# Performance work log

Hardware: AMD Instinct MI355X
Metric: run time of the kernel (lower is better)

Reference implementation:

```python
import jax, jax.numpy as jnp
import numpy as np
from jax import lax

WINDOW_SIZE = 11
SIGMA = 1.5
DATA_RANGE = 1.0


def _gaussian_window(channels):
    coords = jnp.arange(WINDOW_SIZE, dtype=jnp.float32) - WINDOW_SIZE // 2
    g = jnp.exp(-coords ** 2 / (2.0 * SIGMA ** 2))
    g = g / g.sum()
    w2d = jnp.outer(g, g)
    w2d = w2d / w2d.sum()
    # depthwise kernel: (C, 1, K, K) in OIHW with feature_group_count=C
    return jnp.broadcast_to(w2d, (channels, 1, WINDOW_SIZE, WINDOW_SIZE))


def _dwconv(x, window, channels):
    pad = WINDOW_SIZE // 2
    return lax.conv_general_dilated(
        x, window,
        window_strides=(1, 1),
        padding=[(pad, pad), (pad, pad)],
        dimension_numbers=('NCHW', 'OIHW', 'NCHW'),
        feature_group_count=channels,
    )


def setup_inputs() -> dict:
    key = jax.random.key(0)
    k1, k2 = jax.random.split(key)
    B, C, H, W = 16, 3, 512, 512
    x = jax.random.uniform(k1, (B, C, H, W), dtype=jnp.float32)
    y = jax.random.uniform(k2, (B, C, H, W), dtype=jnp.float32)
    return {"x": x, "y": y}


def reference(x, y):
    channels = x.shape[1]
    window = _gaussian_window(channels)
    mu_x = _dwconv(x, window, channels)
    mu_y = _dwconv(y, window, channels)
    mu_x2 = mu_x * mu_x
    mu_y2 = mu_y * mu_y
    mu_xy = mu_x * mu_y
    sigma_x2 = _dwconv(x * x, window, channels) - mu_x2
    sigma_y2 = _dwconv(y * y, window, channels) - mu_y2
    sigma_xy = _dwconv(x * y, window, channels) - mu_xy
    c1 = (0.01 * DATA_RANGE) ** 2
    c2 = (0.03 * DATA_RANGE) ** 2
    ssim_map = (2 * mu_xy + c1) * (2 * sigma_xy + c2) / (
        (mu_x2 + mu_y2 + c1) * (sigma_x2 + sigma_y2 + c2) + 1e-08)
    per_image = ssim_map.mean(axis=(1, 2, 3))
    return 1.0 - per_image.mean()
```

## Files before the change

kernel.cpp:

```cpp
#include <hip/hip_runtime.h>
#include <math.h>


#define IMG_W 512
#define IMG_H 512
#define PLANES 48
#define TX 64
#define TYS 128
#define RAD 5
#define NT 256
#define GDX (IMG_W / TX)
#define GDY (IMG_H / TYS)
#define NBLK (GDX * GDY * PLANES)
#define NWAVES (NBLK * 4)
#define NCH 9
#define CSTR 40
#define PSTR (16 * CSTR)
#define WSTR (4 * PSTR)
#define NUMREC (IMG_W * IMG_H * 4)
#define CHSTEP (16 * IMG_W * 4)
#define INVW  0.26601181f
#define GC2   0.32059890f

typedef _Float16 h2 __attribute__((ext_vector_type(2)));
typedef _Float16 h4 __attribute__((ext_vector_type(4)));
typedef _Float16 h8 __attribute__((ext_vector_type(8)));
typedef float f32x4 __attribute__((ext_vector_type(4)));
typedef int i32x4 __attribute__((ext_vector_type(4)));

__device__ __forceinline__ i32x4 make_srd(const float* p) {
    union { i32x4 v; struct { const float* p; unsigned rng; unsigned cfg; } s; } u;
    u.s.p = p; u.s.rng = NUMREC; u.s.cfg = 0x00020000u;
    return u.v;
}

template<int N>
__device__ __forceinline__ void vwait() {
    asm volatile("s_waitcnt vmcnt(%0)" :: "n"(N) : "memory");
    __builtin_amdgcn_sched_barrier(0);
}

__device__ __forceinline__ float exp2_fast(float a) {
#if __has_builtin(__builtin_amdgcn_exp2f)
    return __builtin_amdgcn_exp2f(a);
#else
    return exp2f(a);
#endif
}

__device__ __forceinline__ float wbandf(int idx) {
    const float fd = (float)(idx - 5);
    const float g = exp2_fast(-(fd * fd) * GC2) * INVW;
    return ((unsigned)idx <= 10u) ? g : 0.f;
}

__device__ __forceinline__ h2 pkrtz(float a, float b) {
    auto t = __builtin_amdgcn_cvt_pkrtz(a, b);
    h2 r;
    __builtin_memcpy(&r, &t, sizeof(r));
    return r;
}

__device__ __forceinline__ h4 pack4(f32x4 a) {
    const h2 lo = pkrtz(a[0], a[1]), hi = pkrtz(a[2], a[3]);
    h4 v;
    v[0] = lo.x; v[1] = lo.y; v[2] = hi.x; v[3] = hi.y;
    return v;
}

__device__ __forceinline__ void hconv_chunk(
    f32x4 xa, f32x4 xb, f32x4 ya, f32x4 yb, h8 whB,
    _Float16* wp)
{
    const f32x4 zz = {0.f, 0.f, 0.f, 0.f};
    const h2 xh0 = pkrtz(xa[0], xa[1]), xh1 = pkrtz(xa[2], xa[3]);
    const h2 xh2 = pkrtz(xb[0], xb[1]), xh3 = pkrtz(xb[2], xb[3]);
    const h2 yh0 = pkrtz(ya[0], ya[1]), yh1 = pkrtz(ya[2], ya[3]);
    const h2 yh2 = pkrtz(yb[0], yb[1]), yh3 = pkrtz(yb[2], yb[3]);
    const h2 s0 = xh0 + yh0, s1 = xh1 + yh1, s2 = xh2 + yh2, s3 = xh3 + yh3;
    const h2 d0 = xh0 - yh0, d1 = xh1 - yh1, d2 = xh2 - yh2, d3 = xh3 - yh3;
    h8 sA, dA;
    sA[0] = s0.x; sA[1] = s0.y; sA[2] = s1.x; sA[3] = s1.y;
    sA[4] = s2.x; sA[5] = s2.y; sA[6] = s3.x; sA[7] = s3.y;
    dA[0] = d0.x; dA[1] = d0.y; dA[2] = d1.x; dA[3] = d1.y;
    dA[4] = d2.x; dA[5] = d2.y; dA[6] = d3.x; dA[7] = d3.y;
    const h8 s2A = sA * sA;
    const h8 d2A = dA * dA;
    const f32x4 hS  = __builtin_amdgcn_mfma_f32_16x16x32_f16(sA,  whB, zz, 0, 0, 0);
    const f32x4 hD  = __builtin_amdgcn_mfma_f32_16x16x32_f16(dA,  whB, zz, 0, 0, 0);
    const f32x4 hS2 = __builtin_amdgcn_mfma_f32_16x16x32_f16(s2A, whB, zz, 0, 0, 0);
    const f32x4 hD2 = __builtin_amdgcn_mfma_f32_16x16x32_f16(d2A, whB, zz, 0, 0, 0);
    *(h4*)(wp + 0 * PSTR) = pack4(hS);
    *(h4*)(wp + 1 * PSTR) = pack4(hD);
    *(h4*)(wp + 2 * PSTR) = pack4(hS2);
    *(h4*)(wp + 3 * PSTR) = pack4(hD2);
}

__device__ __forceinline__ float mapsum(f32x4 aS, f32x4 aD, f32x4 aS2, f32x4 aD2,
                                        float cv)
{
    float local = 0.f;
    #pragma unroll
    for (int r = 0; r < 4; ++r) {
        const float mS = aS[r]  * cv, mD = aD[r]  * cv;
        const float eS = aS2[r] * cv, eD = aD2[r] * cv;
        const float ms2 = mS * mS, md2 = mD * mD;
        const float Pm = 0.5f * (ms2 - md2);
        const float Qm = 0.5f * (ms2 + md2);
        const float Pe = 0.5f * (eS - eD);
        const float Qe = 0.5f * (eS + eD);
        const float c1 = 1e-4f, c2 = 9e-4f;
        const float num = (Pm + c1) * (Pe - Pm + c2);
        const float den = (Qm + c1) * (Qe - Qm + c2) + 1e-8f;
        local += num * __builtin_amdgcn_rcpf(den);
    }
    return local;
}

#define MFMA16(A, B, C) __builtin_amdgcn_mfma_f32_16x16x32_f16((A), (B), (C), 0, 0, 0)

#define ISSUE(slot) do {                                                      \
    asm volatile("buffer_load_dwordx4 %0, %1, %2, 0 offen"                    \
                 : "=v"(LXA[slot]) : "v"(voff), "s"(srdx));                   \
    asm volatile("buffer_load_dwordx4 %0, %1, %2, 0 offen offset:16"          \
                 : "=v"(LXB[slot]) : "v"(voff), "s"(srdx));                   \
    asm volatile("buffer_load_dwordx4 %0, %1, %2, 0 offen"                    \
                 : "=v"(LYA[slot]) : "v"(voff), "s"(srdy));                   \
    asm volatile("buffer_load_dwordx4 %0, %1, %2, 0 offen offset:16"          \
                 : "=v"(LYB[slot]) : "v"(voff), "s"(srdy));                   \
    voff += CHSTEP;                                                           \
} while (0)

#define VCONV(C) do {                                                         \
    const _Float16* rp = rbase + ((((C) + qh) & 1) << 4);                     \
    const h8 B0 = *(const h8*)(rp + 0 * PSTR);           \
    const h8 B1 = *(const h8*)(rp + 1 * PSTR);                                \
    const h8 B2 = *(const h8*)(rp + 2 * PSTR);                                \
    const h8 B3 = *(const h8*)(rp + 3 * PSTR);                                \
    const f32x4 aS  = MFMA16(wvA, B0, zz);                                    \
    const f32x4 aD  = MFMA16(wvA, B1, zz);                                    \
    const f32x4 aS2 = MFMA16(wvA, B2, zz);                                    \
    const f32x4 aD2 = MFMA16(wvA, B3, zz);                                    \
    local += mapsum(aS, aD, aS2, aD2, cv);                                    \
} while (0)

__global__ __launch_bounds__(NT, 4) void ssim_tile_kernel(
    const float* __restrict__ x, const float* __restrict__ y,
    float* __restrict__ partials)
{
    __shared__ __align__(16) _Float16 Ht[4 * WSTR];

    const int tid = threadIdx.x;
    const int l = tid & 63, wid = tid >> 6;
    const int q = l >> 4, fc = l & 15;
    const int ql = q & 1, qh = q >> 1;

    const int plane = blockIdx.z;
    const i32x4 srdx = make_srd(x + (size_t)plane * IMG_H * IMG_W);
    const i32x4 srdy = make_srd(y + (size_t)plane * IMG_H * IMG_W);
    const int C0 = blockIdx.x * TX;
    const int R0 = blockIdx.y * TYS;
    const int c0 = 16 * wid;
    const int gcol = C0 + c0 - 8 + 8 * q;
    int voff = ((unsigned)gcol < (unsigned)IMG_W)
             ? (((R0 - RAD + fc) << 11) + (gcol << 2)) : 0x60000000;

    f32x4 LXA[3], LXB[3], LYA[3], LYB[3];
    ISSUE(0); ISSUE(1); ISSUE(2);

    float s2w = 0.f;
    #pragma unroll
    for (int k = 0; k <= 10; ++k) s2w += (float)(_Float16)wbandf(k);
    const float cv = 1.f / (s2w * s2w);

    h8 whB, wvA;
    #pragma unroll
    for (int e = 0; e < 8; ++e) {
        whB[e] = (_Float16)wbandf(8 * q + e - fc - 3);
        wvA[e] = (_Float16)wbandf(8 * q + e - fc);
    }

    _Float16* const Hw = Ht + wid * WSTR;
    _Float16* const hwr = Hw + fc * CSTR + 4 * q;
    const _Float16* const rbase = Hw + fc * CSTR + 8 * ql;

    const f32x4 zz = {0.f, 0.f, 0.f, 0.f};
    float local = 0.f;

    #pragma unroll
    for (int c = 0; c < NCH; ++c) {
        if (c >= 2) VCONV(c);
        if (c <= 6) vwait<8>();
        else if (c == 7) vwait<4>();
        else vwait<0>();
        hconv_chunk(LXA[c % 3], LXB[c % 3], LYA[c % 3], LYB[c % 3],
                    whB, hwr + ((c & 1) << 4));
        if (c + 3 < NCH) ISSUE(c % 3);
    }

    VCONV(9);

    #pragma unroll
    for (int off = 32; off > 0; off >>= 1)
        local += __shfl_down(local, off, 64);
    const int gid = (blockIdx.x + GDX * (blockIdx.y + GDY * blockIdx.z)) * 4 + wid;
    if (l == 0) partials[gid] = local;
}

__global__ __launch_bounds__(256) void ssim_finalize_kernel(
    const float* __restrict__ partials, float* __restrict__ out)
{
    const int tid = threadIdx.x;
    double s = 0.0;
    #pragma unroll 4
    for (int i = tid; i < NWAVES; i += 256) s += (double)partials[i];
    #pragma unroll
    for (int off = 32; off > 0; off >>= 1)
        s += __shfl_down(s, off, 64);
    __shared__ double ws_[256 / 64];
    const int lane = tid & 63, wv = tid >> 6;
    if (lane == 0) ws_[wv] = s;
    __syncthreads();
    if (tid == 0) {
        const double t = ws_[0] + ws_[1] + ws_[2] + ws_[3];
        const double n = (double)PLANES * IMG_H * IMG_W;
        out[0] = (float)(1.0 - t / n);
    }
}

extern "C" void kernel_launch(void* const* d_in, const int* in_sizes, int n_in,
                              void* d_out, int out_size, void* d_ws, size_t ws_size,
                              hipStream_t stream)
{
    const float* x = (const float*)d_in[0];
    const float* y = (const float*)d_in[1];
    float* out = (float*)d_out;
    float* partials = (float*)d_ws;

    dim3 grid(GDX, GDY, PLANES);
    ssim_tile_kernel<<<grid, NT, 0, stream>>>(x, y, partials);
    ssim_finalize_kernel<<<1, 256, 0, stream>>>(partials, out);
}
```

Before: 131.2 us.

## Fuse final reduction into tile kernel via atomics and last-block finalize

Removes the separate finalize kernel launch. Each block now reduces its four wave sums in shared memory, adds them atomically into a double accumulator, and the last block to finish, found through an atomic counter, writes the output. A memset is added before the launch to zero the accumulator and counter. The global loads also gain an sc0 cache-policy bit. The double atomics add contention and make the summation order nondeterministic, and the memset is an extra stream operation.

```diff
diff --git a/kernel.cpp b/kernel.cpp
--- a/kernel.cpp
+++ b/kernel.cpp
@@ -12,7 +12,6 @@
 #define GDX (IMG_W / TX)
 #define GDY (IMG_H / TYS)
 #define NBLK (GDX * GDY * PLANES)
-#define NWAVES (NBLK * 4)
 #define NCH 9
 #define CSTR 40
 #define PSTR (16 * CSTR)
@@ -120,13 +119,13 @@
 #define MFMA16(A, B, C) __builtin_amdgcn_mfma_f32_16x16x32_f16((A), (B), (C), 0, 0, 0)
 
 #define ISSUE(slot) do {                                                      \
-    asm volatile("buffer_load_dwordx4 %0, %1, %2, 0 offen"                    \
+    asm volatile("buffer_load_dwordx4 %0, %1, %2, 0 offen sc0"                \
                  : "=v"(LXA[slot]) : "v"(voff), "s"(srdx));                   \
-    asm volatile("buffer_load_dwordx4 %0, %1, %2, 0 offen offset:16"          \
+    asm volatile("buffer_load_dwordx4 %0, %1, %2, 0 offen offset:16 sc0"      \
                  : "=v"(LXB[slot]) : "v"(voff), "s"(srdx));                   \
-    asm volatile("buffer_load_dwordx4 %0, %1, %2, 0 offen"                    \
+    asm volatile("buffer_load_dwordx4 %0, %1, %2, 0 offen sc0"                \
                  : "=v"(LYA[slot]) : "v"(voff), "s"(srdy));                   \
-    asm volatile("buffer_load_dwordx4 %0, %1, %2, 0 offen offset:16"          \
+    asm volatile("buffer_load_dwordx4 %0, %1, %2, 0 offen offset:16 sc0"      \
                  : "=v"(LYB[slot]) : "v"(voff), "s"(srdy));                   \
     voff += CHSTEP;                                                           \
 } while (0)
@@ -146,9 +145,11 @@
 
 __global__ __launch_bounds__(NT, 4) void ssim_tile_kernel(
     const float* __restrict__ x, const float* __restrict__ y,
-    float* __restrict__ partials)
+    double* __restrict__ acc, unsigned* __restrict__ cnt,
+    float* __restrict__ out)
 {
     __shared__ __align__(16) _Float16 Ht[4 * WSTR];
+    __shared__ float wave_sums[NT / 64];
 
     const int tid = threadIdx.x;
     const int l = tid & 63, wid = tid >> 6;
@@ -203,28 +204,19 @@
     #pragma unroll
     for (int off = 32; off > 0; off >>= 1)
         local += __shfl_down(local, off, 64);
-    const int gid = (blockIdx.x + GDX * (blockIdx.y + GDY * blockIdx.z)) * 4 + wid;
-    if (l == 0) partials[gid] = local;
-}
-
-__global__ __launch_bounds__(256) void ssim_finalize_kernel(
-    const float* __restrict__ partials, float* __restrict__ out)
-{
-    const int tid = threadIdx.x;
-    double s = 0.0;
-    #pragma unroll 4
-    for (int i = tid; i < NWAVES; i += 256) s += (double)partials[i];
-    #pragma unroll
-    for (int off = 32; off > 0; off >>= 1)
-        s += __shfl_down(s, off, 64);
-    __shared__ double ws_[256 / 64];
-    const int lane = tid & 63, wv = tid >> 6;
-    if (lane == 0) ws_[wv] = s;
+    if (l == 0) wave_sums[wid] = local;
     __syncthreads();
     if (tid == 0) {
-        const double t = ws_[0] + ws_[1] + ws_[2] + ws_[3];
-        const double n = (double)PLANES * IMG_H * IMG_W;
-        out[0] = (float)(1.0 - t / n);
+        const double s = (double)wave_sums[0] + (double)wave_sums[1]
+                       + (double)wave_sums[2] + (double)wave_sums[3];
+        atomicAdd(acc, s);
+        __threadfence();
+        const unsigned t = atomicAdd(cnt, 1u);
+        if (t == NBLK - 1) {
+            const double tot = atomicAdd(acc, 0.0);
+            const double n = (double)PLANES * IMG_H * IMG_W;
+            out[0] = (float)(1.0 - tot / n);
+        }
     }
 }
 
@@ -235,9 +227,11 @@
     const float* x = (const float*)d_in[0];
     const float* y = (const float*)d_in[1];
     float* out = (float*)d_out;
-    float* partials = (float*)d_ws;
+    double* acc = (double*)d_ws;
+    unsigned* cnt = (unsigned*)((char*)d_ws + 8);
+
+    hipMemsetAsync(d_ws, 0, 16, stream);
 
     dim3 grid(GDX, GDY, PLANES);
-    ssim_tile_kernel<<<grid, NT, 0, stream>>>(x, y, partials);
-    ssim_finalize_kernel<<<1, 256, 0, stream>>>(partials, out);
-}
+    ssim_tile_kernel<<<grid, NT, 0, stream>>>(x, y, acc, cnt, out);
+}
```

Result: slower. 196.8 us (+50.0%).

## Stage input tile cooperatively in LDS to remove redundant halo loads

Applied to the files above, without the earlier changes.

Each block now loads its 16-row chunk of x and y (including the column halo) once, cooperatively, into a double-buffered LDS staging area as fp16 sum/difference, instead of each wave loading its own overlapping 32-column slice. The horizontal MFMA pass then reads from LDS. This removes duplicated global loads across the four waves. In exchange it adds a __syncthreads per chunk and drops the three-deep register prefetch to a single chunk in flight, with a full vwait<0> each iteration, which may expose memory latency. Partials are also reduced per block rather than per wave.

```diff
diff --git a/kernel.cpp b/kernel.cpp
--- a/kernel.cpp
+++ b/kernel.cpp
@@ -12,8 +12,9 @@
 #define GDX (IMG_W / TX)
 #define GDY (IMG_H / TYS)
 #define NBLK (GDX * GDY * PLANES)
-#define NWAVES (NBLK * 4)
 #define NCH 9
+#define SC4 20
+#define SSTR 88
 #define CSTR 40
 #define PSTR (16 * CSTR)
 #define WSTR (4 * PSTR)
@@ -66,34 +67,6 @@
     h4 v;
     v[0] = lo.x; v[1] = lo.y; v[2] = hi.x; v[3] = hi.y;
     return v;
-}
-
-__device__ __forceinline__ void hconv_chunk(
-    f32x4 xa, f32x4 xb, f32x4 ya, f32x4 yb, h8 whB,
-    _Float16* wp)
-{
-    const f32x4 zz = {0.f, 0.f, 0.f, 0.f};
-    const h2 xh0 = pkrtz(xa[0], xa[1]), xh1 = pkrtz(xa[2], xa[3]);
-    const h2 xh2 = pkrtz(xb[0], xb[1]), xh3 = pkrtz(xb[2], xb[3]);
-    const h2 yh0 = pkrtz(ya[0], ya[1]), yh1 = pkrtz(ya[2], ya[3]);
-    const h2 yh2 = pkrtz(yb[0], yb[1]), yh3 = pkrtz(yb[2], yb[3]);
-    const h2 s0 = xh0 + yh0, s1 = xh1 + yh1, s2 = xh2 + yh2, s3 = xh3 + yh3;
-    const h2 d0 = xh0 - yh0, d1 = xh1 - yh1, d2 = xh2 - yh2, d3 = xh3 - yh3;
-    h8 sA, dA;
-    sA[0] = s0.x; sA[1] = s0.y; sA[2] = s1.x; sA[3] = s1.y;
-    sA[4] = s2.x; sA[5] = s2.y; sA[6] = s3.x; sA[7] = s3.y;
-    dA[0] = d0.x; dA[1] = d0.y; dA[2] = d1.x; dA[3] = d1.y;
-    dA[4] = d2.x; dA[5] = d2.y; dA[6] = d3.x; dA[7] = d3.y;
-    const h8 s2A = sA * sA;
-    const h8 d2A = dA * dA;
-    const f32x4 hS  = __builtin_amdgcn_mfma_f32_16x16x32_f16(sA,  whB, zz, 0, 0, 0);
-    const f32x4 hD  = __builtin_amdgcn_mfma_f32_16x16x32_f16(dA,  whB, zz, 0, 0, 0);
-    const f32x4 hS2 = __builtin_amdgcn_mfma_f32_16x16x32_f16(s2A, whB, zz, 0, 0, 0);
-    const f32x4 hD2 = __builtin_amdgcn_mfma_f32_16x16x32_f16(d2A, whB, zz, 0, 0, 0);
-    *(h4*)(wp + 0 * PSTR) = pack4(hS);
-    *(h4*)(wp + 1 * PSTR) = pack4(hD);
-    *(h4*)(wp + 2 * PSTR) = pack4(hS2);
-    *(h4*)(wp + 3 * PSTR) = pack4(hD2);
 }
 
 __device__ __forceinline__ float mapsum(f32x4 aS, f32x4 aD, f32x4 aS2, f32x4 aD2,
@@ -119,16 +92,30 @@
 
 #define MFMA16(A, B, C) __builtin_amdgcn_mfma_f32_16x16x32_f16((A), (B), (C), 0, 0, 0)
 
-#define ISSUE(slot) do {                                                      \
+#define ISSUE() do {                                                          \
     asm volatile("buffer_load_dwordx4 %0, %1, %2, 0 offen"                    \
-                 : "=v"(LXA[slot]) : "v"(voff), "s"(srdx));                   \
-    asm volatile("buffer_load_dwordx4 %0, %1, %2, 0 offen offset:16"          \
-                 : "=v"(LXB[slot]) : "v"(voff), "s"(srdx));                   \
+                 : "=v"(X0) : "v"(voff0), "s"(srdx));                         \
     asm volatile("buffer_load_dwordx4 %0, %1, %2, 0 offen"                    \
-                 : "=v"(LYA[slot]) : "v"(voff), "s"(srdy));                   \
-    asm volatile("buffer_load_dwordx4 %0, %1, %2, 0 offen offset:16"          \
-                 : "=v"(LYB[slot]) : "v"(voff), "s"(srdy));                   \
-    voff += CHSTEP;                                                           \
+                 : "=v"(Y0) : "v"(voff0), "s"(srdy));                         \
+    if (has1) {                                                               \
+        asm volatile("buffer_load_dwordx4 %0, %1, %2, 0 offen"                \
+                     : "=v"(X1) : "v"(voff1), "s"(srdx));                     \
+        asm volatile("buffer_load_dwordx4 %0, %1, %2, 0 offen"                \
+                     : "=v"(Y1) : "v"(voff1), "s"(srdy));                     \
+    }                                                                         \
+    voff0 += CHSTEP; voff1 += CHSTEP;                                         \
+} while (0)
+
+#define STAGE_WRITE(X, Y, ROW, C4, SLOT) do {                                 \
+    const h2 xl = pkrtz((X)[0], (X)[1]), xh = pkrtz((X)[2], (X)[3]);          \
+    const h2 yl = pkrtz((Y)[0], (Y)[1]), yh = pkrtz((Y)[2], (Y)[3]);          \
+    const h2 sl = xl + yl, sh = xh + yh;                                      \
+    const h2 dl = xl - yl, dh = xh - yh;                                      \
+    h4 sv, dv;                                                                \
+    sv[0] = sl.x; sv[1] = sl.y; sv[2] = sh.x; sv[3] = sh.y;                   \
+    dv[0] = dl.x; dv[1] = dl.y; dv[2] = dh.x; dv[3] = dh.y;                   \
+    *(h4*)&sdIn[SLOT][0][ROW][4 * (C4)] = sv;                                 \
+    *(h4*)&sdIn[SLOT][1][ROW][4 * (C4)] = dv;                                 \
 } while (0)
 
 #define VCONV(C) do {                                                         \
@@ -148,7 +135,9 @@
     const float* __restrict__ x, const float* __restrict__ y,
     float* __restrict__ partials)
 {
+    __shared__ _Float16 sdIn[2][2][16][SSTR];
     __shared__ __align__(16) _Float16 Ht[4 * WSTR];
+    __shared__ float wave_sums[NT / 64];
 
     const int tid = threadIdx.x;
     const int l = tid & 63, wid = tid >> 6;
@@ -161,12 +150,20 @@
     const int C0 = blockIdx.x * TX;
     const int R0 = blockIdx.y * TYS;
     const int c0 = 16 * wid;
-    const int gcol = C0 + c0 - 8 + 8 * q;
-    int voff = ((unsigned)gcol < (unsigned)IMG_W)
-             ? (((R0 - RAD + fc) << 11) + (gcol << 2)) : 0x60000000;
-
-    f32x4 LXA[3], LXB[3], LYA[3], LYB[3];
-    ISSUE(0); ISSUE(1); ISSUE(2);
+
+    const int row0 = tid / SC4, c40 = tid - SC4 * row0;
+    const bool has1 = tid < 320 - NT;
+    const int p1 = NT + tid;
+    const int row1 = p1 / SC4, c41 = p1 - SC4 * row1;
+    const int gcol0 = C0 - 8 + 4 * c40;
+    const int gcol1 = C0 - 8 + 4 * c41;
+    int voff0 = ((unsigned)gcol0 < (unsigned)IMG_W)
+              ? (((R0 - RAD + row0) << 11) + (gcol0 << 2)) : 0x60000000;
+    int voff1 = ((unsigned)gcol1 < (unsigned)IMG_W)
+              ? (((R0 - RAD + row1) << 11) + (gcol1 << 2)) : 0x60000000;
+
+    f32x4 X0, Y0, X1, Y1;
+    ISSUE();
 
     float s2w = 0.f;
     #pragma unroll
@@ -189,13 +186,29 @@
 
     #pragma unroll
     for (int c = 0; c < NCH; ++c) {
+        vwait<0>();
+        STAGE_WRITE(X0, Y0, row0, c40, c & 1);
+        if (has1) STAGE_WRITE(X1, Y1, row1, c41, c & 1);
+        if (c + 1 < NCH) ISSUE();
+        __syncthreads();
+
         if (c >= 2) VCONV(c);
-        if (c <= 6) vwait<8>();
-        else if (c == 7) vwait<4>();
-        else vwait<0>();
-        hconv_chunk(LXA[c % 3], LXB[c % 3], LYA[c % 3], LYB[c % 3],
-                    whB, hwr + ((c & 1) << 4));
-        if (c + 3 < NCH) ISSUE(c % 3);
+
+        {
+            const h8 sA = *(const h8*)&sdIn[c & 1][0][fc][c0 + 8 * q];
+            const h8 dA = *(const h8*)&sdIn[c & 1][1][fc][c0 + 8 * q];
+            const h8 s2A = sA * sA;
+            const h8 d2A = dA * dA;
+            const f32x4 hS  = MFMA16(sA,  whB, zz);
+            const f32x4 hD  = MFMA16(dA,  whB, zz);
+            const f32x4 hS2 = MFMA16(s2A, whB, zz);
+            const f32x4 hD2 = MFMA16(d2A, whB, zz);
+            _Float16* wp = hwr + ((c & 1) << 4);
+            *(h4*)(wp + 0 * PSTR) = pack4(hS);
+            *(h4*)(wp + 1 * PSTR) = pack4(hD);
+            *(h4*)(wp + 2 * PSTR) = pack4(hS2);
+            *(h4*)(wp + 3 * PSTR) = pack4(hD2);
+        }
     }
 
     VCONV(9);
@@ -203,8 +216,13 @@
     #pragma unroll
     for (int off = 32; off > 0; off >>= 1)
         local += __shfl_down(local, off, 64);
-    const int gid = (blockIdx.x + GDX * (blockIdx.y + GDY * blockIdx.z)) * 4 + wid;
-    if (l == 0) partials[gid] = local;
+    if (l == 0) wave_sums[wid] = local;
+    __syncthreads();
+    if (tid == 0) {
+        const float s = wave_sums[0] + wave_sums[1] + wave_sums[2] + wave_sums[3];
+        const int bid = blockIdx.x + GDX * (blockIdx.y + GDY * blockIdx.z);
+        partials[bid] = s;
+    }
 }
 
 __global__ __launch_bounds__(256) void ssim_finalize_kernel(
@@ -213,7 +231,7 @@
     const int tid = threadIdx.x;
     double s = 0.0;
     #pragma unroll 4
-    for (int i = tid; i < NWAVES; i += 256) s += (double)partials[i];
+    for (int i = tid; i < NBLK; i += 256) s += (double)partials[i];
     #pragma unroll
     for (int off = 32; off > 0; off >>= 1)
         s += __shfl_down(s, off, 64);
```

Measured after the change: 186.0 us. 41.7% more time.

## Double tile height, remap 1D grid across XCDs, reduce partials per block

Applied to the files above, without the earlier changes.

Raises the rows per tile from 128 to 256 (17 chunks instead of 9), so the 10-row vertical halo is amortized over twice as many output rows. The grid becomes 1D with a block-id swizzle that spreads consecutive blocks across the 8 XCDs. Next-chunk loads are now issued before the horizontal convolution, and the four per-wave sums are combined in shared memory so each block writes one partial. The trade-off is half as many blocks (768), which may leave the GPU less well filled and cut latency hiding, plus an extra __syncthreads per block.

```diff
diff --git a/kernel.cpp b/kernel.cpp
--- a/kernel.cpp
+++ b/kernel.cpp
@@ -6,14 +6,13 @@
 #define IMG_H 512
 #define PLANES 48
 #define TX 64
-#define TYS 128
+#define TYS 256
 #define RAD 5
 #define NT 256
 #define GDX (IMG_W / TX)
 #define GDY (IMG_H / TYS)
 #define NBLK (GDX * GDY * PLANES)
-#define NWAVES (NBLK * 4)
-#define NCH 9
+#define NCH 17
 #define CSTR 40
 #define PSTR (16 * CSTR)
 #define WSTR (4 * PSTR)
@@ -149,17 +148,23 @@
     float* __restrict__ partials)
 {
     __shared__ __align__(16) _Float16 Ht[4 * WSTR];
+    __shared__ float wave_sums[NT / 64];
 
     const int tid = threadIdx.x;
     const int l = tid & 63, wid = tid >> 6;
     const int q = l >> 4, fc = l & 15;
     const int ql = q & 1, qh = q >> 1;
 
-    const int plane = blockIdx.z;
+    const int bid = blockIdx.x;
+    const int sid = (bid & 7) * (NBLK / 8) + (bid >> 3);
+    const int plane = sid >> 4;
+    const int rem = sid & 15;
+    const int by = rem >> 3, bx = rem & 7;
+
     const i32x4 srdx = make_srd(x + (size_t)plane * IMG_H * IMG_W);
     const i32x4 srdy = make_srd(y + (size_t)plane * IMG_H * IMG_W);
-    const int C0 = blockIdx.x * TX;
-    const int R0 = blockIdx.y * TYS;
+    const int C0 = bx * TX;
+    const int R0 = by * TYS;
     const int c0 = 16 * wid;
     const int gcol = C0 + c0 - 8 + 8 * q;
     int voff = ((unsigned)gcol < (unsigned)IMG_W)
@@ -190,21 +195,26 @@
     #pragma unroll
     for (int c = 0; c < NCH; ++c) {
         if (c >= 2) VCONV(c);
-        if (c <= 6) vwait<8>();
-        else if (c == 7) vwait<4>();
+        if (c <= NCH - 3) vwait<8>();
+        else if (c == NCH - 2) vwait<4>();
         else vwait<0>();
-        hconv_chunk(LXA[c % 3], LXB[c % 3], LYA[c % 3], LYB[c % 3],
-                    whB, hwr + ((c & 1) << 4));
+        const f32x4 xa = LXA[c % 3], xb = LXB[c % 3];
+        const f32x4 ya = LYA[c % 3], yb = LYB[c % 3];
         if (c + 3 < NCH) ISSUE(c % 3);
-    }
-
-    VCONV(9);
+        hconv_chunk(xa, xb, ya, yb, whB, hwr + ((c & 1) << 4));
+    }
+
+    VCONV(NCH);
 
     #pragma unroll
     for (int off = 32; off > 0; off >>= 1)
         local += __shfl_down(local, off, 64);
-    const int gid = (blockIdx.x + GDX * (blockIdx.y + GDY * blockIdx.z)) * 4 + wid;
-    if (l == 0) partials[gid] = local;
+    if (l == 0) wave_sums[wid] = local;
+    __syncthreads();
+    if (tid == 0) {
+        const float s = wave_sums[0] + wave_sums[1] + wave_sums[2] + wave_sums[3];
+        partials[bid] = s;
+    }
 }
 
 __global__ __launch_bounds__(256) void ssim_finalize_kernel(
@@ -213,7 +223,7 @@
     const int tid = threadIdx.x;
     double s = 0.0;
     #pragma unroll 4
-    for (int i = tid; i < NWAVES; i += 256) s += (double)partials[i];
+    for (int i = tid; i < NBLK; i += 256) s += (double)partials[i];
     #pragma unroll
     for (int off = 32; off > 0; off >>= 1)
         s += __shfl_down(s, off, 64);
@@ -237,7 +247,6 @@
     float* out = (float*)d_out;
     float* partials = (float*)d_ws;
 
-    dim3 grid(GDX, GDY, PLANES);
-    ssim_tile_kernel<<<grid, NT, 0, stream>>>(x, y, partials);
+    ssim_tile_kernel<<<dim3(NBLK, 1, 1), NT, 0, stream>>>(x, y, partials);
     ssim_finalize_kernel<<<1, 256, 0, stream>>>(partials, out);
 }
```

Result: no change. 131.1 us (-0.1%).
